# Optimization experiments

Measured on AMD Instinct MI355X. Metric: run time of the kernel, lower is better.

The kernel has to match this reference:

```python
import jax, jax.numpy as jnp
import numpy as np

def setup_inputs() -> dict:
    key = jax.random.key(0)
    k1, k2, k3 = jax.random.split(key, 3)
    N, C, H, W = 16, 128, 128, 128
    out_chn = 128
    x = jax.random.normal(k1, (N, C, H, W), dtype=jnp.float32)
    # 1x1 conv = per-pixel linear: weight (out_chn, in_chn), bias (out_chn,)
    fan_in = C  # kernel_size=1 -> fan_in = in_chn
    bound = 1.0 / np.sqrt(fan_in)
    conv_w = jax.random.uniform(k2, (out_chn, C), dtype=jnp.float32, minval=-bound, maxval=bound)
    conv_b = jax.random.uniform(k3, (out_chn,), dtype=jnp.float32, minval=-bound, maxval=bound)
    return {"x": x, "conv_w": conv_w, "conv_b": conv_b}

def reference(x, conv_w, conv_b):
    N, C, H, W = x.shape
    x_hw = x.reshape(N, C, H * W)                     # (N, C, HW)
    logits = jnp.einsum('ncl,ndl->ncd', x_hw, x_hw)    # (N, C, C), unscaled
    weights = jax.nn.softmax(logits, axis=-1)
    attn = jnp.einsum('ncd,ndl->ncl', weights, x_hw)   # (N, C, HW)
    attn = attn.reshape(N, C, H, W)
    # 1x1 conv: contract over channel dim
    out = jnp.einsum('nchw,oc->nohw', attn, conv_w) + conv_b[None, :, None, None]
    return out
```

## Files before the change

### kernel.cpp

```cpp
#include <hip/hip_runtime.h>
#include <hip/hip_bf16.h>
#include <stdint.h>

#define NB    16
#define CD    128
#define HW    16384

typedef float  f32x4  __attribute__((ext_vector_type(4)));
typedef short  bf16x8 __attribute__((ext_vector_type(8)));

__device__ __forceinline__ unsigned f2bf(float f) {
    unsigned u = __float_as_uint(f);
    u += 0x7FFFu + ((u >> 16) & 1u);
    return u >> 16;
}

__global__ __launch_bounds__(256) void gram_kernel(const float* __restrict__ x,
                                                   float* __restrict__ G) {
    const int n  = blockIdx.x;
    const int kc = blockIdx.y;
    const int t    = threadIdx.x;
    const int wv   = t >> 6;
    const int lane = t & 63;
    const int q    = lane >> 4;
    const int r16  = lane & 15;

    __shared__ __align__(16) unsigned short Xl[CD * 132];

    f32x4 acc[4][4];
#pragma unroll
    for (int i = 0; i < 4; ++i)
#pragma unroll
        for (int j = 0; j < 4; ++j) acc[i][j] = (f32x4)0.0f;

    const int rt0 = 4 * (wv >> 1);
    const int ct0 = 4 * (wv & 1);

    const float* xb = x + (size_t)n * CD * HW;

    for (int sub = 0; sub < 2; ++sub) {
        const int kbase = kc * 256 + sub * 128;
#pragma unroll
        for (int i = 0; i < 16; ++i) {
            int f  = i * 256 + t;
            int c  = f >> 5;
            int l4 = (f & 31) * 4;
            float4 v = *(const float4*)(xb + (size_t)c * HW + kbase + l4);
            uint2 pk;
            pk.x = f2bf(v.x) | (f2bf(v.y) << 16);
            pk.y = f2bf(v.z) | (f2bf(v.w) << 16);
            *(uint2*)(&Xl[c * 132 + l4]) = pk;
        }
        __syncthreads();

#pragma unroll
        for (int ks = 0; ks < 4; ++ks) {
            const int k0 = ks * 32 + q * 8;
            bf16x8 af[4], bfr[4];
#pragma unroll
            for (int i = 0; i < 4; ++i) {
                const unsigned short* pa = &Xl[(16 * (rt0 + i) + r16) * 132 + k0];
                union { bf16x8 v; uint2 u[2]; } ua;
                ua.u[0] = *(const uint2*)pa;
                ua.u[1] = *(const uint2*)(pa + 4);
                af[i] = ua.v;
                const unsigned short* pb = &Xl[(16 * (ct0 + i) + r16) * 132 + k0];
                union { bf16x8 v; uint2 u[2]; } ub;
                ub.u[0] = *(const uint2*)pb;
                ub.u[1] = *(const uint2*)(pb + 4);
                bfr[i] = ub.v;
            }
#pragma unroll
            for (int i = 0; i < 4; ++i)
#pragma unroll
                for (int j = 0; j < 4; ++j)
                    acc[i][j] = __builtin_amdgcn_mfma_f32_16x16x32_bf16(
                        af[i], bfr[j], acc[i][j], 0, 0, 0);
        }
        __syncthreads();
    }

    float* Gn = G + (size_t)n * CD * CD;
#pragma unroll
    for (int i = 0; i < 4; ++i)
#pragma unroll
        for (int j = 0; j < 4; ++j)
#pragma unroll
            for (int rr = 0; rr < 4; ++rr) {
                int row = 16 * (rt0 + i) + q * 4 + rr;
                int col = 16 * (ct0 + j) + r16;
                atomicAdd(&Gn[row * CD + col], acc[i][j][rr]);
            }
}

__global__ __launch_bounds__(256) void rowstats_kernel(const float* __restrict__ G,
                                                       float* __restrict__ mx,
                                                       float* __restrict__ rs) {
    const int row  = blockIdx.x * 4 + (threadIdx.x >> 6);
    const int lane = threadIdx.x & 63;
    const float* g = G + (size_t)row * CD;
    float g0 = g[lane];
    float g1 = g[lane + 64];
    float m = fmaxf(g0, g1);
#pragma unroll
    for (int off = 32; off > 0; off >>= 1) m = fmaxf(m, __shfl_xor(m, off));
    float s = __expf(g0 - m) + __expf(g1 - m);
#pragma unroll
    for (int off = 32; off > 0; off >>= 1) s += __shfl_xor(s, off);
    if (lane == 0) {
        mx[row] = m;
        rs[row] = 1.0f / s;
    }
}

__global__ __launch_bounds__(256) void mmat_kernel(const float* __restrict__ G,
                                                   const float* __restrict__ mx,
                                                   const float* __restrict__ rs,
                                                   const float* __restrict__ cw,
                                                   unsigned short* __restrict__ Mbf) {
    const int n  = blockIdx.x;
    const int bo = blockIdx.y;
    const int t  = threadIdx.x;
    __shared__ __align__(16) float Wl[CD * CD];

    const float* Gn  = G  + (size_t)n * CD * CD;
    const float* mxn = mx + n * CD;
    const float* rsn = rs + n * CD;

#pragma unroll 4
    for (int i = 0; i < 64; ++i) {
        int e = i * 256 + t;
        int c = e >> 7;
        int d = e & 127;
        Wl[c * CD + d] = __expf(Gn[c * CD + d] - mxn[c]) * rsn[c];
    }
    __syncthreads();

    const int o  = bo * 16 + (t >> 4);
    const int d0 = (t & 15) * 8;
    float a0 = 0, a1 = 0, a2 = 0, a3 = 0, a4 = 0, a5 = 0, a6 = 0, a7 = 0;
    const float* cwo = cw + (size_t)o * CD;
#pragma unroll 4
    for (int c = 0; c < CD; ++c) {
        float cv = cwo[c];
        float4 w0 = *(const float4*)&Wl[c * CD + d0];
        float4 w1 = *(const float4*)&Wl[c * CD + d0 + 4];
        a0 += cv * w0.x; a1 += cv * w0.y; a2 += cv * w0.z; a3 += cv * w0.w;
        a4 += cv * w1.x; a5 += cv * w1.y; a6 += cv * w1.z; a7 += cv * w1.w;
    }
    uint4 pk;
    pk.x = f2bf(a0) | (f2bf(a1) << 16);
    pk.y = f2bf(a2) | (f2bf(a3) << 16);
    pk.z = f2bf(a4) | (f2bf(a5) << 16);
    pk.w = f2bf(a6) | (f2bf(a7) << 16);
    *(uint4*)&Mbf[((size_t)n * CD + o) * CD + d0] = pk;
}

__global__ __launch_bounds__(256) void out_kernel(const float* __restrict__ x,
                                                  const unsigned short* __restrict__ Mbf,
                                                  const float* __restrict__ bias,
                                                  float* __restrict__ out) {
    const int lb = blockIdx.x;
    const int n  = blockIdx.y;
    const int l0 = lb * 128;
    const int t    = threadIdx.x;
    const int wv   = t >> 6;
    const int lane = t & 63;
    const int q    = lane >> 4;
    const int r16  = lane & 15;

    __shared__ __align__(16) unsigned short Xt[128 * 128];
    __shared__ float bl[CD];

    const int lt0 = 4 * (wv >> 1);
    const int ot0 = 4 * (wv & 1);

    if (t < CD) bl[t] = bias[t];

    const float* xb = x + (size_t)n * CD * HW + l0;
    const int lt = t & 31;
    const int dg = t >> 5;
#pragma unroll
    for (int i = 0; i < 4; ++i) {
        const int d0 = i * 32 + dg * 4;
        const float* bp = xb + (size_t)d0 * HW + 4 * lt;
        float4 v0 = *(const float4*)(bp);
        float4 v1 = *(const float4*)(bp + HW);
        float4 v2 = *(const float4*)(bp + 2 * HW);
        float4 v3 = *(const float4*)(bp + 3 * HW);
        float r0[4] = {v0.x, v0.y, v0.z, v0.w};
        float r1[4] = {v1.x, v1.y, v1.z, v1.w};
        float r2[4] = {v2.x, v2.y, v2.z, v2.w};
        float r3[4] = {v3.x, v3.y, v3.z, v3.w};
        const int dph = d0 ^ (8 * (lt & 7));
#pragma unroll
        for (int j = 0; j < 4; ++j) {
            uint2 pk;
            pk.x = f2bf(r0[j]) | (f2bf(r1[j]) << 16);
            pk.y = f2bf(r2[j]) | (f2bf(r3[j]) << 16);
            *(uint2*)&Xt[(4 * lt + j) * 128 + dph] = pk;
        }
    }
    __syncthreads();

    f32x4 acc[4][4];
#pragma unroll
    for (int i = 0; i < 4; ++i)
#pragma unroll
        for (int j = 0; j < 4; ++j) acc[i][j] = (f32x4)0.0f;

    const unsigned short* Mn = Mbf + (size_t)n * CD * CD;
#pragma unroll
    for (int ks = 0; ks < 4; ++ks) {
        const int k0 = ks * 32 + q * 8;
        bf16x8 bfr[4];
#pragma unroll
        for (int j = 0; j < 4; ++j) {
            const int o = 16 * (ot0 + j) + r16;
            union { bf16x8 v; uint4 u; } ub;
            ub.u = *(const uint4*)&Mn[o * CD + k0];
            bfr[j] = ub.v;
        }
        bf16x8 af[4];
#pragma unroll
        for (int i = 0; i < 4; ++i) {
            const int l = 16 * (lt0 + i) + r16;
            const int doff = k0 ^ (8 * ((l >> 2) & 7));
            union { bf16x8 v; uint4 u; } ua;
            ua.u = *(const uint4*)&Xt[l * 128 + doff];
            af[i] = ua.v;
        }
#pragma unroll
        for (int i = 0; i < 4; ++i)
#pragma unroll
            for (int j = 0; j < 4; ++j)
                acc[i][j] = __builtin_amdgcn_mfma_f32_16x16x32_bf16(
                    af[i], bfr[j], acc[i][j], 0, 0, 0);
    }

    float* ob = out + (size_t)n * CD * HW + l0;
#pragma unroll
    for (int i = 0; i < 4; ++i)
#pragma unroll
        for (int j = 0; j < 4; ++j) {
            const int o = 16 * (ot0 + j) + r16;
            const int l = 16 * (lt0 + i) + q * 4;
            const float b = bl[o];
            float4 st;
            st.x = acc[i][j][0] + b;
            st.y = acc[i][j][1] + b;
            st.z = acc[i][j][2] + b;
            st.w = acc[i][j][3] + b;
            *(float4*)(ob + (size_t)o * HW + l) = st;
        }
}

extern "C" void kernel_launch(void* const* d_in, const int* in_sizes, int n_in,
                              void* d_out, int out_size, void* d_ws, size_t ws_size,
                              hipStream_t stream) {
    const float* x  = (const float*)d_in[0];
    const float* cw = (const float*)d_in[1];
    const float* cb = (const float*)d_in[2];
    float* out = (float*)d_out;

    char* ws = (char*)d_ws;
    float*          G   = (float*)(ws);
    float*          mxp = (float*)(ws + (1u << 20));
    float*          rsp = (float*)(ws + (1u << 20) + 8192);
    unsigned short* Mbf = (unsigned short*)(ws + (1u << 20) + 16384);

    hipMemsetAsync(G, 0, (size_t)NB * CD * CD * sizeof(float), stream);

    gram_kernel    <<<dim3(NB, 64), 256, 0, stream>>>(x, G);
    rowstats_kernel<<<dim3(512),    256, 0, stream>>>(G, mxp, rsp);
    mmat_kernel    <<<dim3(NB, 8),  256, 0, stream>>>(G, mxp, rsp, cw, Mbf);
    out_kernel     <<<dim3(128, NB), 256, 0, stream>>>(x, Mbf, cb, out);
}
```

Before: 340.9 us.

## Replace atomic Gram accumulation with split-K partials and a fused reduce pass

The Gram kernel now writes per-K-chunk partial results to a 32-slice workspace with plain stores instead of atomicAdd into a zeroed G. The memset is removed, and the row-stats kernel becomes a reduce kernel that sums the partials, writes G, and computes softmax max and sum. K chunks double in size, so the block count halves (16x32). This removes atomic contention and the memset launch, but adds 32MB of partial writes and reads and lowers parallelism in the Gram kernel.

```diff
diff --git a/kernel.cpp b/kernel.cpp
--- a/kernel.cpp
+++ b/kernel.cpp
@@ -5,6 +5,7 @@
 #define NB    16
 #define CD    128
 #define HW    16384
+#define KSPLIT 32
 
 typedef float  f32x4  __attribute__((ext_vector_type(4)));
 typedef short  bf16x8 __attribute__((ext_vector_type(8)));
@@ -16,7 +17,7 @@
 }
 
 __global__ __launch_bounds__(256) void gram_kernel(const float* __restrict__ x,
-                                                   float* __restrict__ G) {
+                                                   float* __restrict__ P) {
     const int n  = blockIdx.x;
     const int kc = blockIdx.y;
     const int t    = threadIdx.x;
@@ -38,8 +39,8 @@
 
     const float* xb = x + (size_t)n * CD * HW;
 
-    for (int sub = 0; sub < 2; ++sub) {
-        const int kbase = kc * 256 + sub * 128;
+    for (int sub = 0; sub < 4; ++sub) {
+        const int kbase = kc * 512 + sub * 128;
 #pragma unroll
         for (int i = 0; i < 16; ++i) {
             int f  = i * 256 + t;
@@ -80,7 +81,7 @@
         __syncthreads();
     }
 
-    float* Gn = G + (size_t)n * CD * CD;
+    float* Pn = P + ((size_t)kc * NB + n) * CD * CD;
 #pragma unroll
     for (int i = 0; i < 4; ++i)
 #pragma unroll
@@ -89,27 +90,40 @@
             for (int rr = 0; rr < 4; ++rr) {
                 int row = 16 * (rt0 + i) + q * 4 + rr;
                 int col = 16 * (ct0 + j) + r16;
-                atomicAdd(&Gn[row * CD + col], acc[i][j][rr]);
+                Pn[row * CD + col] = acc[i][j][rr];
             }
 }
 
-__global__ __launch_bounds__(256) void rowstats_kernel(const float* __restrict__ G,
-                                                       float* __restrict__ mx,
-                                                       float* __restrict__ rs) {
-    const int row  = blockIdx.x * 4 + (threadIdx.x >> 6);
+__global__ __launch_bounds__(256) void reduce_kernel(const float* __restrict__ P,
+                                                     float* __restrict__ G,
+                                                     float* __restrict__ mx,
+                                                     float* __restrict__ rs) {
+    const int R    = blockIdx.x * 4 + (threadIdx.x >> 6);
     const int lane = threadIdx.x & 63;
-    const float* g = G + (size_t)row * CD;
-    float g0 = g[lane];
-    float g1 = g[lane + 64];
-    float m = fmaxf(g0, g1);
+    const int n    = R >> 7;
+    const int row  = R & 127;
+
+    const float* p = P + (size_t)n * CD * CD + (size_t)row * CD;
+    float s0 = 0.0f, s1 = 0.0f;
+#pragma unroll
+    for (int kc = 0; kc < KSPLIT; ++kc) {
+        const float* pk = p + (size_t)kc * NB * CD * CD;
+        s0 += pk[lane];
+        s1 += pk[lane + 64];
+    }
+    float m = fmaxf(s0, s1);
 #pragma unroll
     for (int off = 32; off > 0; off >>= 1) m = fmaxf(m, __shfl_xor(m, off));
-    float s = __expf(g0 - m) + __expf(g1 - m);
-#pragma unroll
-    for (int off = 32; off > 0; off >>= 1) s += __shfl_xor(s, off);
+    float e = __expf(s0 - m) + __expf(s1 - m);
+#pragma unroll
+    for (int off = 32; off > 0; off >>= 1) e += __shfl_xor(e, off);
+
+    float* g = G + (size_t)n * CD * CD + (size_t)row * CD;
+    g[lane]      = s0;
+    g[lane + 64] = s1;
     if (lane == 0) {
-        mx[row] = m;
-        rs[row] = 1.0f / s;
+        mx[R] = m;
+        rs[R] = 1.0f / e;
     }
 }
 
@@ -264,15 +278,14 @@
     float* out = (float*)d_out;
 
     char* ws = (char*)d_ws;
-    float*          G   = (float*)(ws);
-    float*          mxp = (float*)(ws + (1u << 20));
-    float*          rsp = (float*)(ws + (1u << 20) + 8192);
-    unsigned short* Mbf = (unsigned short*)(ws + (1u << 20) + 16384);
-
-    hipMemsetAsync(G, 0, (size_t)NB * CD * CD * sizeof(float), stream);
-
-    gram_kernel    <<<dim3(NB, 64), 256, 0, stream>>>(x, G);
-    rowstats_kernel<<<dim3(512),    256, 0, stream>>>(G, mxp, rsp);
-    mmat_kernel    <<<dim3(NB, 8),  256, 0, stream>>>(G, mxp, rsp, cw, Mbf);
-    out_kernel     <<<dim3(128, NB), 256, 0, stream>>>(x, Mbf, cb, out);
-}
+    float*          P   = (float*)(ws);
+    float*          G   = (float*)(ws + (32u << 20));
+    float*          mxp = (float*)(ws + (33u << 20));
+    float*          rsp = (float*)(ws + (33u << 20) + 8192);
+    unsigned short* Mbf = (unsigned short*)(ws + (33u << 20) + 16384);
+
+    gram_kernel   <<<dim3(NB, KSPLIT), 256, 0, stream>>>(x, P);
+    reduce_kernel <<<dim3(512),        256, 0, stream>>>(P, G, mxp, rsp);
+    mmat_kernel   <<<dim3(NB, 8),      256, 0, stream>>>(G, mxp, rsp, cw, Mbf);
+    out_kernel    <<<dim3(128, NB),    256, 0, stream>>>(x, Mbf, cb, out);
+}
```

After: 303.3 us. 1.12x faster.
